# Kernel optimization log

Hardware: AMD Instinct MI355X
Metric: run time of the kernel (lower is better)

Reference implementation:

```python
import jax, jax.numpy as jnp
import numpy as np

B, S, R, E, H = 2, 256, 2048, 1024, 16
D = E // H
ROPE_BASE = 10000.0

_PN = ["sum_q", "sum_k", "sum_v", "sum_out", "reg_q", "reg_k", "reg_v", "reg_out", "sum_k2", "sum_v2"]


def setup_inputs() -> dict:
    key = jax.random.key(0)
    ks = jax.random.split(key, 2 + 2 * len(_PN))
    inp = {
        "sum_x": jax.random.normal(ks[0], (B, S, E), jnp.float32),
        "reg_x": jax.random.normal(ks[1], (B, R, E), jnp.float32),
        "ss_mask": jnp.ones((B, S, S), bool),
        "sr_mask": jnp.ones((B, S, R), bool),
        "rs_mask": jnp.ones((B, R, S), bool),
        "rr_mask": jnp.ones((B, R, R), bool),
    }
    for i, n in enumerate(_PN):
        inp[f"W_{n}"] = jax.random.normal(ks[2 + 2 * i], (E, E), jnp.float32) * 0.02
        inp[f"b_{n}"] = jax.random.normal(ks[3 + 2 * i], (E,), jnp.float32) * 0.02
    return inp


def _lin(x, W, b):
    return x @ W.T + b


def _heads(x):  # (B, L, E) -> (B, H, L, D)
    b, l, _ = x.shape
    return x.reshape(b, l, H, D).transpose(0, 2, 1, 3)


def _merge(x):  # (B, H, L, D) -> (B, L, E)
    b, _, l, _ = x.shape
    return x.transpose(0, 2, 1, 3).reshape(b, l, E)


def _rope_cos_sin(total_len):
    inv_freq = 1.0 / (ROPE_BASE ** (jnp.arange(0, D, 2, dtype=jnp.float32) / D))
    t = jnp.arange(total_len, dtype=jnp.float32)
    freqs = jnp.outer(t, inv_freq)
    emb = jnp.concatenate([freqs, freqs], axis=-1)  # (total_len, D)
    return jnp.cos(emb)[None, None], jnp.sin(emb)[None, None]


def _rotate_half(x):
    x1, x2 = jnp.split(x, 2, axis=-1)
    return jnp.concatenate([-x2, x1], axis=-1)


def _apply_rope(q, k, cos, sin):
    return q * cos + _rotate_half(q) * sin, k * cos + _rotate_half(k) * sin


def _attn(q, k, v, mask):  # mask: (B, Lq, Lk) bool
    scale = D ** -0.5
    scores = jnp.einsum('bhqd,bhkd->bhqk', q, k) * scale
    scores = jnp.where(mask[:, None, :, :], scores, -jnp.inf)
    p = jax.nn.softmax(scores, axis=-1)
    return jnp.einsum('bhqk,bhkd->bhqd', p, v)


def summary_attention(sum_x, reg_x, ss_mask, sr_mask, rs_mask, rr_mask, params):
    sum_len, reg_len = sum_x.shape[1], reg_x.shape[1]
    sum_q = _heads(_lin(sum_x, params["W_sum_q"], params["b_sum_q"]))
    sum_k = _heads(_lin(sum_x, params["W_sum_k"], params["b_sum_k"]))
    sum_v = _heads(_lin(sum_x, params["W_sum_v"], params["b_sum_v"]))
    reg_q = _heads(_lin(reg_x, params["W_reg_q"], params["b_reg_q"]))
    reg_k = _heads(_lin(reg_x, params["W_reg_k"], params["b_reg_k"]))
    reg_v = _heads(_lin(reg_x, params["W_reg_v"], params["b_reg_v"]))

    cos, sin = _rope_cos_sin(sum_len + reg_len)
    sum_q, sum_k = _apply_rope(sum_q, sum_k, cos[:, :, :sum_len], sin[:, :, :sum_len])
    reg_q, reg_k = _apply_rope(reg_q, reg_k, cos[:, :, sum_len:], sin[:, :, sum_len:])

    # Stage 1: summary queries over [summary, regular] keys
    src_k = jnp.concatenate([sum_k, reg_k], axis=2)
    src_v = jnp.concatenate([sum_v, reg_v], axis=2)
    sx_mask = jnp.concatenate([ss_mask, sr_mask], axis=-1)
    sum_attn_out = _merge(_attn(sum_q, src_k, src_v, sx_mask))  # (B, S, E)

    # Second projection of summarized tokens
    sum_k2 = _heads(_lin(sum_attn_out, params["W_sum_k2"], params["b_sum_k2"]))
    sum_v2 = _heads(_lin(sum_attn_out, params["W_sum_v2"], params["b_sum_v2"]))

    # Stage 2: regular queries over [summary2, regular] keys
    src_k2 = jnp.concatenate([sum_k2, reg_k], axis=2)
    src_v2 = jnp.concatenate([sum_v2, reg_v], axis=2)
    rx_mask = jnp.concatenate([rs_mask, rr_mask], axis=-1)
    reg_attn_out = _merge(_attn(reg_q, src_k2, src_v2, rx_mask))  # (B, R, E)

    sum_output = _lin(sum_attn_out, params["W_sum_out"], params["b_sum_out"])
    reg_output = _lin(reg_attn_out, params["W_reg_out"], params["b_reg_out"])
    return sum_output, reg_output


def reference(sum_x, reg_x, ss_mask, sr_mask, rs_mask, rr_mask,
              W_sum_q, b_sum_q, W_sum_k, b_sum_k, W_sum_v, b_sum_v,
              W_sum_out, b_sum_out, W_reg_q, b_reg_q, W_reg_k, b_reg_k,
              W_reg_v, b_reg_v, W_reg_out, b_reg_out, W_sum_k2, b_sum_k2,
              W_sum_v2, b_sum_v2):
    params = dict(W_sum_q=W_sum_q, b_sum_q=b_sum_q, W_sum_k=W_sum_k, b_sum_k=b_sum_k,
                  W_sum_v=W_sum_v, b_sum_v=b_sum_v, W_sum_out=W_sum_out, b_sum_out=b_sum_out,
                  W_reg_q=W_reg_q, b_reg_q=b_reg_q, W_reg_k=W_reg_k, b_reg_k=b_reg_k,
                  W_reg_v=W_reg_v, b_reg_v=b_reg_v, W_reg_out=W_reg_out, b_reg_out=b_reg_out,
                  W_sum_k2=W_sum_k2, b_sum_k2=b_sum_k2, W_sum_v2=W_sum_v2, b_sum_v2=b_sum_v2)
    return summary_attention(sum_x, reg_x, ss_mask, sr_mask, rs_mask, rr_mask, params)
```

## Files before the change

### kernel.cpp

```cpp
#include <hip/hip_runtime.h>
#include <math.h>

#define SUMSZ 524288
#define REGSZ 4194304
#define CSCALE 0.18033688f

typedef unsigned short us;
typedef __attribute__((ext_vector_type(8))) short short8;
typedef __attribute__((ext_vector_type(4))) float f32x4;

__device__ __forceinline__ us f2bf(float f) {
    unsigned u = __builtin_bit_cast(unsigned, f);
    u += 0x7FFF + ((u >> 16) & 1);
    return (us)(u >> 16);
}
__device__ __forceinline__ float fast_exp2(float x) {
    return __builtin_amdgcn_exp2f(x);
}
__device__ __forceinline__ unsigned pack_trunc(float a, float b, float& qa, float& qb) {
    unsigned ua = __builtin_bit_cast(unsigned, a);
    unsigned ub = __builtin_bit_cast(unsigned, b);
    qa = __builtin_bit_cast(float, ua & 0xffff0000u);
    qb = __builtin_bit_cast(float, ub & 0xffff0000u);
    return (ub & 0xffff0000u) | (ua >> 16);
}

typedef const __attribute__((address_space(1))) unsigned int gu32;
typedef __attribute__((address_space(3))) unsigned int lu32;
__device__ __forceinline__ void gld16(const us* g, us* l) {
    __builtin_amdgcn_global_load_lds((gu32*)g, (lu32*)l, 16, 0, 0);
}

struct GArgs {
    const us* A0; const us* A1;
    const us* W[6]; const float* bias[6]; void* C[6];
    int flag[6];
    int rope[6];
    float scale[6];
    const float* tab;
    int xsplit, Lmask0, Lmask1;
};

template<int BM>
__global__ __launch_bounds__(256) void gemm6_kernel(GArgs a)
{
    constexpr int TI = (BM == 128) ? 4 : 2;
    const int tid = threadIdx.x;
    const int l = tid & 63, w = tid >> 6;
    const int col = l & 15, g = l >> 4;
    const int wm = w >> 1, wn = w & 1;
    const int part = (blockIdx.x >= a.xsplit) ? 1 : 0;
    const int m0 = (part ? (blockIdx.x - a.xsplit) : blockIdx.x) * BM;
    const us* A = part ? a.A1 : a.A0;
    const int Lmask = part ? a.Lmask1 : a.Lmask0;
    const int nG = blockIdx.y * 128;
    const int set = part * 3 + (nG >> 10);
    const int n0 = nG & 1023;
    const us* W = a.W[set];
    const float* bias = a.bias[set];
    void* C = a.C[set];
    const int flag = a.flag[set];
    const int rope = a.rope[set];
    const float scl = a.scale[set];
    const float* tab = a.tab;

    __shared__ us As[2][(BM / 16) * 512];
    __shared__ us Bs[2][4096];

    f32x4 acc[TI][4];
    #pragma unroll
    for (int i = 0; i < TI; ++i)
        #pragma unroll
        for (int j = 0; j < 4; ++j) acc[i][j] = (f32x4){0.f, 0.f, 0.f, 0.f};

    const us* ga = A + (size_t)(m0 + w * 16 + col) * 1024 + g * 8;
    const us* gb = W + (size_t)(n0 + w * 16 + col) * 1024 + g * 8;

    auto stage = [&](int bi, int kt) {
        gld16(ga + kt, &As[bi][w * 512]);
        if constexpr (BM == 128) gld16(ga + 65536 + kt, &As[bi][(w + 4) * 512]);
        gld16(gb + kt, &Bs[bi][w * 512]);
        gld16(gb + 65536 + kt, &Bs[bi][(w + 4) * 512]);
    };
    stage(0, 0);

    int buf = 0;
    for (int kt = 0; kt < 1024; kt += 32) {
        __syncthreads();
        if (kt + 32 < 1024) stage(buf ^ 1, kt + 32);

        short8 af[TI], bfr[4];
        #pragma unroll
        for (int i = 0; i < TI; ++i) af[i]  = *(const short8*)&As[buf][(wm * TI + i) * 512 + l * 8];
        #pragma unroll
        for (int j = 0; j < 4; ++j) bfr[j] = *(const short8*)&Bs[buf][(wn * 4 + j) * 512 + l * 8];
        #pragma unroll
        for (int i = 0; i < TI; ++i)
            #pragma unroll
            for (int j = 0; j < 4; ++j)
                acc[i][j] = __builtin_amdgcn_mfma_f32_16x16x32_bf16(af[i], bfr[j], acc[i][j], 0, 0, 0);
        buf ^= 1;
    }

    float bv0 = bias[n0 + wn * 64 +  0 + col];
    float bv1 = bias[n0 + wn * 64 + 16 + col];
    float bv2 = bias[n0 + wn * 64 + 32 + col];
    float bv3 = bias[n0 + wn * 64 + 48 + col];
    #pragma unroll
    for (int i = 0; i < TI; ++i) {
        #pragma unroll
        for (int r = 0; r < 4; ++r) {
            int row = m0 + wm * (TI * 16) + i * 16 + g * 4 + r;
            float a0 = acc[i][0][r] + bv0;
            float a1 = acc[i][1][r] + bv1;
            float a2 = acc[i][2][r] + bv2;
            float a3 = acc[i][3][r] + bv3;
            if (rope >= 0) {
                int pos = (row & Lmask) + rope;
                float c0 = tab[(pos * 32 + col) * 2],      s0 = tab[(pos * 32 + col) * 2 + 1];
                float c1 = tab[(pos * 32 + col + 16) * 2], s1 = tab[(pos * 32 + col + 16) * 2 + 1];
                float n0v = a0 * c0 - a2 * s0;
                float n1v = a1 * c1 - a3 * s1;
                float n2v = a2 * c0 + a0 * s0;
                float n3v = a3 * c1 + a1 * s1;
                a0 = n0v; a1 = n1v; a2 = n2v; a3 = n3v;
            }
            a0 *= scl; a1 *= scl; a2 *= scl; a3 *= scl;
            size_t base = (size_t)row * 1024 + n0 + wn * 64 + col;
            if (flag) {
                us* Ch = (us*)C;
                Ch[base]      = f2bf(a0);
                Ch[base + 16] = f2bf(a1);
                Ch[base + 32] = f2bf(a2);
                Ch[base + 48] = f2bf(a3);
            } else {
                float* Cf = (float*)C;
                Cf[base] = a0; Cf[base + 16] = a1; Cf[base + 32] = a2; Cf[base + 48] = a3;
            }
        }
    }
}

__global__ __launch_bounds__(256) void vtrans2_kernel(
    const us* __restrict__ src0, us* __restrict__ dst0, int L0, int xsplit,
    const us* __restrict__ src1, us* __restrict__ dst1, int L1)
{
    const int part = (blockIdx.x >= xsplit) ? 1 : 0;
    const int t = part ? (blockIdx.x - xsplit) : blockIdx.x;
    const us* src = part ? src1 : src0;
    us* dst = part ? dst1 : dst0;
    const int L = part ? L1 : L0;
    const int h = blockIdx.y, b = blockIdx.z;
    __shared__ us T[64][72];
    const int tid = threadIdx.x;
    {
        int key = tid >> 2, seg = (tid & 3) * 16;
        const us* sp = src + ((size_t)b * L + t * 64 + key) * 1024 + h * 64 + seg;
        short8 v0 = *(const short8*)sp;
        short8 v1 = *(const short8*)(sp + 8);
        int kp = (key & 15) * 4 + (key >> 4);
        #pragma unroll
        for (int j = 0; j < 8; ++j) {
            T[seg + j][kp]     = (us)v0[j];
            T[seg + 8 + j][kp] = (us)v1[j];
        }
    }
    __syncthreads();
    {
        int d = tid >> 2, ks = (tid & 3) * 16;
        us* dp = dst + (((size_t)(b * 16 + h) * 64) + d) * L + t * 64 + ks;
        *(short8*)dp       = *(const short8*)&T[d][ks];
        *(short8*)(dp + 8) = *(const short8*)&T[d][ks + 8];
    }
}

template<int NQ, int SPLIT>
__global__ __launch_bounds__(256) void attn5_kernel(
    const us* __restrict__ Q,
    const us* __restrict__ K1, const us* __restrict__ Vt1, int L1,
    const us* __restrict__ K2, const us* __restrict__ Vt2, int L2,
    us* __restrict__ O, float* __restrict__ PO, float* __restrict__ PL, int Lq)
{
    const int tid = threadIdx.x;
    const int l = tid & 63, w = tid >> 6;
    const int col = l & 15, g = l >> 4;
    const int h = blockIdx.y, b = blockIdx.z;
    const int split = blockIdx.x & (SPLIT - 1);
    const int qt = blockIdx.x / SPLIT;

    __shared__ us Ks[2][8 * 512];
    __shared__ us Vs[2][8 * 512];
    __shared__ us Ps[4][NQ * 16 * 72];

    const int rowbase = qt * (NQ * 64) + w * (NQ * 16);

    short8 aq[NQ][2];
    #pragma unroll
    for (int qi = 0; qi < NQ; ++qi) {
        const us* qp = Q + ((size_t)b * Lq + rowbase + qi * 16 + col) * 1024 + h * 64 + g * 8;
        aq[qi][0] = *(const short8*)qp;
        aq[qi][1] = *(const short8*)(qp + 32);
    }

    f32x4 o[NQ][4];
    float lsum[NQ][4];
    #pragma unroll
    for (int qi = 0; qi < NQ; ++qi)
        #pragma unroll
        for (int u = 0; u < 4; ++u) { o[qi][u] = (f32x4){0.f,0.f,0.f,0.f}; lsum[qi][u] = 0.f; }

    const int nt1 = L1 >> 6;
    const int ntt = nt1 + (L2 >> 6);
    const int tpb = ntt / SPLIT;
    const int t0 = split * tpb, t1 = t0 + tpb;

    auto stage = [&](int bi, int t) {
        const us *Kg, *Vg; int Lv, kb;
        if (t < nt1) {
            Kg = K1 + ((size_t)b * L1 + t * 64) * 1024 + h * 64;
            Vg = Vt1 + (size_t)(b * 16 + h) * 64 * L1;
            Lv = L1; kb = t * 64;
        } else {
            Kg = K2 + ((size_t)b * L2 + (t - nt1) * 64) * 1024 + h * 64;
            Vg = Vt2 + (size_t)(b * 16 + h) * 64 * L2;
            Lv = L2; kb = (t - nt1) * 64;
        }
        const us* gp = Kg + (size_t)(w * 16 + col) * 1024 + g * 8;
        gld16(gp,      &Ks[bi][(w * 2 + 0) * 512]);
        gld16(gp + 32, &Ks[bi][(w * 2 + 1) * 512]);
        const us* vp = Vg + (size_t)(w * 16 + col) * Lv + kb + g * 8;
        gld16(vp,      &Vs[bi][(w * 2 + 0) * 512]);
        gld16(vp + 32, &Vs[bi][(w * 2 + 1) * 512]);
    };
    stage(0, t0);

    int buf = 0;
    for (int t = t0; t < t1; ++t) {
        __syncthreads();
        if (t + 1 < t1) stage(buf ^ 1, t + 1);

        short8 kf[8], vb[8];
        #pragma unroll
        for (int f = 0; f < 8; ++f) kf[f] = *(const short8*)&Ks[buf][f * 512 + l * 8];
        #pragma unroll
        for (int f = 0; f < 8; ++f) vb[f] = *(const short8*)&Vs[buf][f * 512 + l * 8];

        #pragma unroll
        for (int qi = 0; qi < NQ; ++qi) {
            f32x4 s0 = {0.f,0.f,0.f,0.f}, s1 = s0, s2 = s0, s3 = s0;
            s0 = __builtin_amdgcn_mfma_f32_16x16x32_bf16(aq[qi][0], kf[0], s0, 0, 0, 0);
            s0 = __builtin_amdgcn_mfma_f32_16x16x32_bf16(aq[qi][1], kf[1], s0, 0, 0, 0);
            s1 = __builtin_amdgcn_mfma_f32_16x16x32_bf16(aq[qi][0], kf[2], s1, 0, 0, 0);
            s1 = __builtin_amdgcn_mfma_f32_16x16x32_bf16(aq[qi][1], kf[3], s1, 0, 0, 0);
            s2 = __builtin_amdgcn_mfma_f32_16x16x32_bf16(aq[qi][0], kf[4], s2, 0, 0, 0);
            s2 = __builtin_amdgcn_mfma_f32_16x16x32_bf16(aq[qi][1], kf[5], s2, 0, 0, 0);
            s3 = __builtin_amdgcn_mfma_f32_16x16x32_bf16(aq[qi][0], kf[6], s3, 0, 0, 0);
            s3 = __builtin_amdgcn_mfma_f32_16x16x32_bf16(aq[qi][1], kf[7], s3, 0, 0, 0);

            #pragma unroll
            for (int r = 0; r < 4; ++r) {
                float p0 = fast_exp2(s0[r]);
                float p1 = fast_exp2(s1[r]);
                float p2 = fast_exp2(s2[r]);
                float p3 = fast_exp2(s3[r]);
                float q0, q1, q2, q3;
                uint2 pkk;
                pkk.x = pack_trunc(p0, p1, q0, q1);
                pkk.y = pack_trunc(p2, p3, q2, q3);
                lsum[qi][r] += (q0 + q1) + (q2 + q3);
                *(uint2*)&Ps[w][(qi * 16 + g * 4 + r) * 72 + col * 4] = pkk;
            }
        }

        #pragma unroll
        for (int qi = 0; qi < NQ; ++qi) {
            short8 ap0 = *(const short8*)&Ps[w][(qi * 16 + col) * 72 + g * 8];
            short8 ap1 = *(const short8*)&Ps[w][(qi * 16 + col) * 72 + 32 + g * 8];
            o[qi][0] = __builtin_amdgcn_mfma_f32_16x16x32_bf16(ap0, vb[0], o[qi][0], 0, 0, 0);
            o[qi][0] = __builtin_amdgcn_mfma_f32_16x16x32_bf16(ap1, vb[1], o[qi][0], 0, 0, 0);
            o[qi][1] = __builtin_amdgcn_mfma_f32_16x16x32_bf16(ap0, vb[2], o[qi][1], 0, 0, 0);
            o[qi][1] = __builtin_amdgcn_mfma_f32_16x16x32_bf16(ap1, vb[3], o[qi][1], 0, 0, 0);
            o[qi][2] = __builtin_amdgcn_mfma_f32_16x16x32_bf16(ap0, vb[4], o[qi][2], 0, 0, 0);
            o[qi][2] = __builtin_amdgcn_mfma_f32_16x16x32_bf16(ap1, vb[5], o[qi][2], 0, 0, 0);
            o[qi][3] = __builtin_amdgcn_mfma_f32_16x16x32_bf16(ap0, vb[6], o[qi][3], 0, 0, 0);
            o[qi][3] = __builtin_amdgcn_mfma_f32_16x16x32_bf16(ap1, vb[7], o[qi][3], 0, 0, 0);
        }
        buf ^= 1;
    }

    #pragma unroll
    for (int qi = 0; qi < NQ; ++qi)
        #pragma unroll
        for (int r = 0; r < 4; ++r) {
            float v = lsum[qi][r];
            v += __shfl_xor(v, 1);
            v += __shfl_xor(v, 2);
            v += __shfl_xor(v, 4);
            v += __shfl_xor(v, 8);
            lsum[qi][r] = v;
        }

    if (SPLIT == 1) {
        #pragma unroll
        for (int qi = 0; qi < NQ; ++qi)
            #pragma unroll
            for (int r = 0; r < 4; ++r) {
                float inv = 1.0f / lsum[qi][r];
                size_t off = ((size_t)b * Lq + rowbase + qi * 16 + g * 4 + r) * 1024 + h * 64 + col;
                O[off]      = f2bf(o[qi][0][r] * inv);
                O[off + 16] = f2bf(o[qi][1][r] * inv);
                O[off + 32] = f2bf(o[qi][2][r] * inv);
                O[off + 48] = f2bf(o[qi][3][r] * inv);
            }
    } else {
        float* po = PO + (size_t)split * ((size_t)2 * Lq * 1024);
        float* pl = PL + split * (2 * Lq * 16);
        #pragma unroll
        for (int qi = 0; qi < NQ; ++qi)
            #pragma unroll
            for (int r = 0; r < 4; ++r) {
                int qr = rowbase + qi * 16 + g * 4 + r;
                size_t off = ((size_t)b * Lq + qr) * 1024 + h * 64 + col;
                po[off]      = o[qi][0][r];
                po[off + 16] = o[qi][1][r];
                po[off + 32] = o[qi][2][r];
                po[off + 48] = o[qi][3][r];
                if (col == 0) pl[(b * Lq + qr) * 16 + h] = lsum[qi][r];
            }
    }
}

__global__ __launch_bounds__(256) void combine_kernel(const float* __restrict__ po,
    const float* __restrict__ pl, us* __restrict__ out)
{
    int idx = blockIdx.x * 256 + threadIdx.x;
    int row = idx >> 10, c = idx & 1023, h = c >> 6;
    float lv = 0.f, ov = 0.f;
    #pragma unroll
    for (int s = 0; s < 4; ++s) {
        lv += pl[s * 8192 + row * 16 + h];
        ov += po[s * 524288 + idx];
    }
    out[idx] = f2bf(ov / lv);
}

__global__ __launch_bounds__(256) void cvt_flat_kernel(
    const float* s0, const float* s1, const float* s2, const float* s3,
    const float* s4, const float* s5, const float* s6, const float* s7,
    const float* s8, const float* s9, const float* s10, const float* s11,
    us* __restrict__ dst, float* __restrict__ tab)
{
    if (blockIdx.x >= 14848) {
        int idx = (blockIdx.x - 14848) * 256 + threadIdx.x;
        int pos = idx >> 5, j = idx & 31;
        float invf = fast_exp2((float)j * -0.41524101f);
        float ang = (float)pos * invf;
        float s, c;
        sincosf(ang, &s, &c);
        tab[idx * 2]     = c;
        tab[idx * 2 + 1] = s;
        return;
    }
    size_t e = (size_t)blockIdx.x * 1024 + threadIdx.x * 4;
    const float* src;
    size_t off;
    if (e < 10485760) {
        const float* ws[10] = {s0,s1,s2,s3,s4,s5,s6,s7,s8,s9};
        src = ws[e >> 20]; off = e & 1048575;
    } else if (e < 11010048) {
        src = s10; off = e - 10485760;
    } else {
        src = s11; off = e - 11010048;
    }
    float4 v = *(const float4*)(src + off);
    us o[4] = {f2bf(v.x), f2bf(v.y), f2bf(v.z), f2bf(v.w)};
    *(uint2*)(dst + e) = *(uint2*)o;
}

extern "C" void kernel_launch(void* const* d_in, const int* in_sizes, int n_in,
                              void* d_out, int out_size, void* d_ws, size_t ws_size,
                              hipStream_t stream)
{
    (void)in_sizes; (void)n_in; (void)out_size; (void)ws_size;

    const float* sum_x_f  = (const float*)d_in[0];
    const float* reg_x_f  = (const float*)d_in[1];
    const float* W_sum_q  = (const float*)d_in[6];  const float* b_sum_q  = (const float*)d_in[7];
    const float* W_sum_k  = (const float*)d_in[8];  const float* b_sum_k  = (const float*)d_in[9];
    const float* W_sum_v  = (const float*)d_in[10]; const float* b_sum_v  = (const float*)d_in[11];
    const float* W_sum_out= (const float*)d_in[12]; const float* b_sum_out= (const float*)d_in[13];
    const float* W_reg_q  = (const float*)d_in[14]; const float* b_reg_q  = (const float*)d_in[15];
    const float* W_reg_k  = (const float*)d_in[16]; const float* b_reg_k  = (const float*)d_in[17];
    const float* W_reg_v  = (const float*)d_in[18]; const float* b_reg_v  = (const float*)d_in[19];
    const float* W_reg_out= (const float*)d_in[20]; const float* b_reg_out= (const float*)d_in[21];
    const float* W_sum_k2 = (const float*)d_in[22]; const float* b_sum_k2 = (const float*)d_in[23];
    const float* W_sum_v2 = (const float*)d_in[24]; const float* b_sum_v2 = (const float*)d_in[25];

    float* out0 = (float*)d_out;
    float* out1 = out0 + SUMSZ;

    us* ws16     = (us*)d_ws;
    us* Wh       = ws16;
    us* xsh      = Wh + 10485760;
    us* xrh      = xsh + SUMSZ;
    us* sum_q    = xrh + REGSZ;
    us* sum_k    = sum_q + SUMSZ;
    us* sum_v    = sum_k + SUMSZ;
    us* sum_attn = sum_v + SUMSZ;
    us* sum_k2   = sum_attn + SUMSZ;
    us* sum_v2   = sum_k2 + SUMSZ;
    us* reg_q    = sum_v2 + SUMSZ;
    us* reg_k    = reg_q + REGSZ;
    us* reg_v    = reg_k + REGSZ;
    us* reg_attn = reg_v + REGSZ;
    us* VtS1     = reg_attn + REGSZ;
    float* tab   = (float*)(VtS1 + SUMSZ);
    float* po    = tab + 147456;
    float* pl    = po + 4 * 524288;
    us* VtR      = xrh;
    us* VtS2     = (us*)po;

    cvt_flat_kernel<<<15136, 256, 0, stream>>>(
        W_sum_q, W_sum_k, W_sum_v, W_sum_out, W_reg_q, W_reg_k, W_reg_v, W_reg_out,
        W_sum_k2, W_sum_v2, sum_x_f, reg_x_f, ws16, tab);

    {
        GArgs a{};
        a.A0 = xsh; a.A1 = xrh; a.xsplit = 4; a.Lmask0 = 255; a.Lmask1 = 2047;
        a.tab = tab;
        a.W[0] = Wh + 0u*1048576; a.bias[0] = b_sum_q; a.C[0] = sum_q; a.flag[0] = 1; a.rope[0] = 0;   a.scale[0] = 1.0f;
        a.W[1] = Wh + 1u*1048576; a.bias[1] = b_sum_k; a.C[1] = sum_k; a.flag[1] = 1; a.rope[1] = 0;   a.scale[1] = CSCALE;
        a.W[2] = Wh + 2u*1048576; a.bias[2] = b_sum_v; a.C[2] = sum_v; a.flag[2] = 1; a.rope[2] = -1;  a.scale[2] = 1.0f;
        a.W[3] = Wh + 4u*1048576; a.bias[3] = b_reg_q; a.C[3] = reg_q; a.flag[3] = 1; a.rope[3] = 256; a.scale[3] = 1.0f;
        a.W[4] = Wh + 5u*1048576; a.bias[4] = b_reg_k; a.C[4] = reg_k; a.flag[4] = 1; a.rope[4] = 256; a.scale[4] = CSCALE;
        a.W[5] = Wh + 6u*1048576; a.bias[5] = b_reg_v; a.C[5] = reg_v; a.flag[5] = 1; a.rope[5] = -1;  a.scale[5] = 1.0f;
        gemm6_kernel<128><<<dim3(36, 24), 256, 0, stream>>>(a);
    }

    vtrans2_kernel<<<dim3(36, 16, 2), 256, 0, stream>>>(
        sum_v, VtS1, 256, 4, reg_v, VtR, 2048);

    attn5_kernel<2, 4><<<dim3(8, 16, 2), 256, 0, stream>>>(
        sum_q, sum_k, VtS1, 256, reg_k, VtR, 2048, nullptr, po, pl, 256);
    combine_kernel<<<2048, 256, 0, stream>>>(po, pl, sum_attn);

    {
        GArgs a{};
        a.A0 = sum_attn; a.A1 = sum_attn; a.xsplit = 8; a.Lmask0 = 255; a.Lmask1 = 255;
        a.tab = tab;
        a.W[0] = Wh + 8u*1048576; a.bias[0] = b_sum_k2; a.C[0] = sum_k2; a.flag[0] = 1; a.rope[0] = -1; a.scale[0] = CSCALE;
        a.W[1] = Wh + 9u*1048576; a.bias[1] = b_sum_v2; a.C[1] = sum_v2; a.flag[1] = 1; a.rope[1] = -1; a.scale[1] = 1.0f;
        a.W[2] = Wh + 3u*1048576; a.bias[2] = b_sum_out;a.C[2] = out0;   a.flag[2] = 0; a.rope[2] = -1; a.scale[2] = 1.0f;
        a.W[3] = a.W[0]; a.bias[3] = a.bias[0]; a.C[3] = a.C[0]; a.flag[3] = 1; a.rope[3] = -1; a.scale[3] = 1.0f;
        a.W[4] = a.W[0]; a.bias[4] = a.bias[0]; a.C[4] = a.C[0]; a.flag[4] = 1; a.rope[4] = -1; a.scale[4] = 1.0f;
        a.W[5] = a.W[0]; a.bias[5] = a.bias[0]; a.C[5] = a.C[0]; a.flag[5] = 1; a.rope[5] = -1; a.scale[5] = 1.0f;
        gemm6_kernel<64><<<dim3(8, 24), 256, 0, stream>>>(a);
    }

    vtrans2_kernel<<<dim3(4, 16, 2), 256, 0, stream>>>(
        sum_v2, VtS2, 256, 4, sum_v2, VtS2, 256);

    attn5_kernel<2, 1><<<dim3(16, 16, 2), 256, 0, stream>>>(
        reg_q, sum_k2, VtS2, 256, reg_k, VtR, 2048, reg_attn, nullptr, nullptr, 2048);

    {
        GArgs a{};
        a.A0 = reg_attn; a.A1 = reg_attn; a.xsplit = 64; a.Lmask0 = 2047; a.Lmask1 = 2047;
        a.tab = tab;
        a.W[0] = Wh + 7u*1048576; a.bias[0] = b_reg_out; a.C[0] = out1; a.flag[0] = 0; a.rope[0] = -1; a.scale[0] = 1.0f;
        for (int s = 1; s < 6; ++s) {
            a.W[s] = a.W[0]; a.bias[s] = a.bias[0]; a.C[s] = a.C[0];
            a.flag[s] = 0; a.rope[s] = -1; a.scale[s] = 1.0f;
        }
        gemm6_kernel<64><<<dim3(64, 8), 256, 0, stream>>>(a);
    }
}
```

Baseline: 391.4 us.

## Triple-buffer GEMM and attention tiles with explicit vmcnt waits

Both the projection GEMM and the attention kernel move from double to triple-buffered LDS staging. Loads are issued two tiles ahead, and __syncthreads is replaced by explicit s_waitcnt vmcnt(N) plus s_barrier, so only the oldest tile's loads are waited on. This lets global-to-LDS transfers overlap more compute. The cost is 50% more LDS per block, which may reduce occupancy, and hand-tuned vmcnt counts that must match the number of loads issued per stage.

```diff
diff --git a/kernel.cpp b/kernel.cpp
--- a/kernel.cpp
+++ b/kernel.cpp
@@ -30,6 +30,10 @@
 __device__ __forceinline__ void gld16(const us* g, us* l) {
     __builtin_amdgcn_global_load_lds((gu32*)g, (lu32*)l, 16, 0, 0);
 }
+
+#define WAIT_VM4_LGKM0 asm volatile("s_waitcnt vmcnt(4) lgkmcnt(0)" ::: "memory")
+#define WAIT_VM3_LGKM0 asm volatile("s_waitcnt vmcnt(3) lgkmcnt(0)" ::: "memory")
+#define WAIT_VM0_LGKM0 asm volatile("s_waitcnt vmcnt(0) lgkmcnt(0)" ::: "memory")
 
 struct GArgs {
     const us* A0; const us* A1;
@@ -64,8 +68,8 @@
     const float scl = a.scale[set];
     const float* tab = a.tab;
 
-    __shared__ us As[2][(BM / 16) * 512];
-    __shared__ us Bs[2][4096];
+    __shared__ us As[3][(BM / 16) * 512];
+    __shared__ us Bs[3][4096];
 
     f32x4 acc[TI][4];
     #pragma unroll
@@ -83,23 +87,32 @@
         gld16(gb + 65536 + kt, &Bs[bi][(w + 4) * 512]);
     };
     stage(0, 0);
-
-    int buf = 0;
+    stage(1, 32);
+
+    int bi = 0;
     for (int kt = 0; kt < 1024; kt += 32) {
-        __syncthreads();
-        if (kt + 32 < 1024) stage(buf ^ 1, kt + 32);
+        if (kt < 992) {
+            if constexpr (BM == 128) WAIT_VM4_LGKM0; else WAIT_VM3_LGKM0;
+        } else {
+            WAIT_VM0_LGKM0;
+        }
+        __builtin_amdgcn_sched_barrier(0);
+        __builtin_amdgcn_s_barrier();
+
+        int bn = bi + 2; if (bn >= 3) bn -= 3;
+        if (kt + 64 < 1024) stage(bn, kt + 64);
 
         short8 af[TI], bfr[4];
         #pragma unroll
-        for (int i = 0; i < TI; ++i) af[i]  = *(const short8*)&As[buf][(wm * TI + i) * 512 + l * 8];
-        #pragma unroll
-        for (int j = 0; j < 4; ++j) bfr[j] = *(const short8*)&Bs[buf][(wn * 4 + j) * 512 + l * 8];
+        for (int i = 0; i < TI; ++i) af[i]  = *(const short8*)&As[bi][(wm * TI + i) * 512 + l * 8];
+        #pragma unroll
+        for (int j = 0; j < 4; ++j) bfr[j] = *(const short8*)&Bs[bi][(wn * 4 + j) * 512 + l * 8];
         #pragma unroll
         for (int i = 0; i < TI; ++i)
             #pragma unroll
             for (int j = 0; j < 4; ++j)
                 acc[i][j] = __builtin_amdgcn_mfma_f32_16x16x32_bf16(af[i], bfr[j], acc[i][j], 0, 0, 0);
-        buf ^= 1;
+        bi = (bi + 1 == 3) ? 0 : bi + 1;
     }
 
     float bv0 = bias[n0 + wn * 64 +  0 + col];
@@ -188,8 +201,8 @@
     const int split = blockIdx.x & (SPLIT - 1);
     const int qt = blockIdx.x / SPLIT;
 
-    __shared__ us Ks[2][8 * 512];
-    __shared__ us Vs[2][8 * 512];
+    __shared__ us Ks[3][8 * 512];
+    __shared__ us Vs[3][8 * 512];
     __shared__ us Ps[4][NQ * 16 * 72];
 
     const int rowbase = qt * (NQ * 64) + w * (NQ * 16);
@@ -233,17 +246,23 @@
         gld16(vp + 32, &Vs[bi][(w * 2 + 1) * 512]);
     };
     stage(0, t0);
-
-    int buf = 0;
+    stage(1, t0 + 1);
+
+    int bi = 0;
     for (int t = t0; t < t1; ++t) {
-        __syncthreads();
-        if (t + 1 < t1) stage(buf ^ 1, t + 1);
+        if (t + 1 < t1) WAIT_VM4_LGKM0;
+        else            WAIT_VM0_LGKM0;
+        __builtin_amdgcn_sched_barrier(0);
+        __builtin_amdgcn_s_barrier();
+
+        int bn = bi + 2; if (bn >= 3) bn -= 3;
+        if (t + 2 < t1) stage(bn, t + 2);
 
         short8 kf[8], vb[8];
         #pragma unroll
-        for (int f = 0; f < 8; ++f) kf[f] = *(const short8*)&Ks[buf][f * 512 + l * 8];
-        #pragma unroll
-        for (int f = 0; f < 8; ++f) vb[f] = *(const short8*)&Vs[buf][f * 512 + l * 8];
+        for (int f = 0; f < 8; ++f) kf[f] = *(const short8*)&Ks[bi][f * 512 + l * 8];
+        #pragma unroll
+        for (int f = 0; f < 8; ++f) vb[f] = *(const short8*)&Vs[bi][f * 512 + l * 8];
 
         #pragma unroll
         for (int qi = 0; qi < NQ; ++qi) {
@@ -285,7 +304,7 @@
             o[qi][3] = __builtin_amdgcn_mfma_f32_16x16x32_bf16(ap0, vb[6], o[qi][3], 0, 0, 0);
             o[qi][3] = __builtin_amdgcn_mfma_f32_16x16x32_bf16(ap1, vb[7], o[qi][3], 0, 0, 0);
         }
-        buf ^= 1;
+        bi = (bi + 1 == 3) ? 0 : bi + 1;
     }
 
     #pragma unroll
```

New measurement: 395.9 us. No clear change (+1.2%).
